# Optimization experiments

Measured on AMD Instinct MI355X. Metric: run time of the kernel, lower is better.

## Reference

```python
import jax, jax.numpy as jnp
import numpy as np

BS, S, D, H, KVH, HD = 2, 2048, 2048, 32, 8, 64
N_REP = H // KVH
N_DOCS = 4


def setup_inputs() -> dict:
    key = jax.random.key(0)
    ks = jax.random.split(key, 7)
    x = jax.random.normal(ks[0], (BS, S, D), dtype=jnp.float32)
    # RoPE table (llama theta=10000), stored as real (cos, sin) pairs: [S, HD//2, 2]
    inv_freq = 1.0 / (10000.0 ** (jnp.arange(0, HD, 2, dtype=jnp.float32) / HD))
    ang = jnp.arange(S, dtype=jnp.float32)[:, None] * inv_freq[None, :]  # [S, HD//2]
    freqs_cis = jnp.stack([jnp.cos(ang), jnp.sin(ang)], axis=-1)
    # packed-document ids, non-decreasing along sequence: [BS, S]
    sequence_id = jnp.sort(
        jax.random.randint(ks[1], (BS, S), 0, N_DOCS, dtype=jnp.int32), axis=-1
    )
    std = 0.02
    wq = jax.random.normal(ks[2], (H * HD, D), dtype=jnp.float32) * std
    wk = jax.random.normal(ks[3], (KVH * HD, D), dtype=jnp.float32) * std
    wv = jax.random.normal(ks[4], (KVH * HD, D), dtype=jnp.float32) * std
    wo = jax.random.normal(ks[5], (D, H * HD), dtype=jnp.float32) * std
    return {"x": x, "freqs_cis": freqs_cis, "sequence_id": sequence_id,
            "wq": wq, "wk": wk, "wv": wv, "wo": wo}


def _apply_rope(t, freqs_cis):
    # t: [b, s, h, hd]; freqs_cis: [s, hd//2, 2] (cos, sin)
    b, s, h, hd = t.shape
    tp = t.reshape(b, s, h, hd // 2, 2)
    t0, t1 = tp[..., 0], tp[..., 1]
    cos = freqs_cis[None, :, None, :, 0]
    sin = freqs_cis[None, :, None, :, 1]
    o0 = t0 * cos - t1 * sin
    o1 = t0 * sin + t1 * cos
    return jnp.stack([o0, o1], axis=-1).reshape(b, s, h, hd)


def reference(x, freqs_cis, sequence_id, wq, wk, wv, wo):
    bs, s, _ = x.shape
    xq = (x @ wq.T).reshape(bs, s, H, HD)
    xk = (x @ wk.T).reshape(bs, s, KVH, HD)
    xv = (x @ wv.T).reshape(bs, s, KVH, HD)
    xq = _apply_rope(xq, freqs_cis)
    xk = _apply_rope(xk, freqs_cis)
    # GQA without materializing repeated KV: group queries by kv head
    q = xq.reshape(bs, s, KVH, N_REP, HD).transpose(0, 2, 3, 1, 4)  # [b,g,r,s,d]
    k = xk.transpose(0, 2, 1, 3)  # [b,g,s,d]
    v = xv.transpose(0, 2, 1, 3)  # [b,g,s,d]
    scale = 1.0 / jnp.sqrt(jnp.float32(HD))
    scores = jnp.einsum("bgrqd,bgkd->bgrqk", q, k) * scale
    # document-causal mask: same sequence_id AND causal
    causal = jnp.tril(jnp.ones((s, s), dtype=bool))
    same_doc = sequence_id[:, :, None] == sequence_id[:, None, :]  # [b,s,s]
    mask = (causal[None] & same_doc)[:, None, None, :, :]  # [b,1,1,s,s]
    scores = jnp.where(mask, scores, jnp.float32(-1e30))
    probs = jax.nn.softmax(scores, axis=-1)
    out = jnp.einsum("bgrqk,bgkd->bgrqd", probs, v)  # [b,g,r,s,d]
    out = out.transpose(0, 3, 1, 2, 4).reshape(bs, s, H * HD)
    return out @ wo.T
```

## Files before the change

kernel.cpp:

```cpp
#include <hip/hip_runtime.h>
#include <hip/hip_bf16.h>

typedef __attribute__((ext_vector_type(8))) short bf16x8;
typedef __attribute__((ext_vector_type(4))) float f32x4;

#define MFMA16(A, B, C) __builtin_amdgcn_mfma_f32_16x16x32_bf16(A, B, C, 0, 0, 0)

__device__ __forceinline__ unsigned short f2bf(float f) {
    unsigned int u = __float_as_uint(f);
    u += 0x7fffu + ((u >> 16) & 1u);
    return (unsigned short)(u >> 16);
}
__device__ __forceinline__ float bf2f(unsigned short h) {
    return __uint_as_float(((unsigned int)h) << 16);
}
__device__ __forceinline__ unsigned int pack_bf2(float lo, float hi) {
    __hip_bfloat162 h = __float22bfloat162_rn(make_float2(lo, hi));
    return *reinterpret_cast<unsigned int*>(&h);
}

__device__ __forceinline__ void gload_lds16(const void* g, void* l) {
    __builtin_amdgcn_global_load_lds(
        (__attribute__((address_space(1))) unsigned int*)g,
        (__attribute__((address_space(3))) unsigned int*)l, 16, 0, 0);
}

__device__ __forceinline__ int swz128(int by) {
    return by ^ (((by >> 7) & 7) << 4);
}

__global__ void cvt_all_kernel(const float* __restrict__ x,  const float* __restrict__ wq,
                               const float* __restrict__ wk, const float* __restrict__ wv,
                               const float* __restrict__ wo,
                               unsigned short* __restrict__ xb,
                               unsigned short* __restrict__ wqkv,
                               unsigned short* __restrict__ wob) {
    const int i = blockIdx.x * 256 + threadIdx.x;
    const float* src;
    unsigned short* dst;
    int off;
    if (i < 2097152)      { src = x;  dst = xb;   off = i; }
    else if (i < 3145728) { src = wq; dst = wqkv; off = i - 2097152; }
    else if (i < 3407872) { src = wk; dst = wqkv + (size_t)2048 * 2048; off = i - 3145728; }
    else if (i < 3670016) { src = wv; dst = wqkv + (size_t)2560 * 2048; off = i - 3407872; }
    else                  { src = wo; dst = wob;  off = i - 3670016; }
    const float4 v = ((const float4*)src)[off];
    uint2 o;
    o.x = pack_bf2(v.x, v.y);
    o.y = pack_bf2(v.z, v.w);
    ((uint2*)dst)[off] = o;
}

__global__ void docstart_kernel(const int* __restrict__ sid, int* __restrict__ ds) {
    const int i = blockIdx.x * 256 + threadIdx.x;
    const int b = i >> 11, s = i & 2047;
    const int* row = sid + b * 2048;
    const int v = row[s];
    int lo = 0, hi = s;
    while (lo < hi) { const int mid = (lo + hi) >> 1; if (row[mid] < v) lo = mid + 1; else hi = mid; }
    ds[i] = lo;
}

#define QKV_K 2048
#define QKV_NT 32
__global__ __launch_bounds__(512, 2) void gemm_qkv8(
    const unsigned short* __restrict__ A,
    const unsigned short* __restrict__ B,
    unsigned short* __restrict__ oq,
    unsigned short* __restrict__ ok,
    unsigned short* __restrict__ ov)
{
    __shared__ __align__(16) unsigned short S[2][2][2][8192];
    const int tid = threadIdx.x, lane = tid & 63, w = tid >> 6;
    const int wr = w >> 2, wc = w & 3;
    const int lr = lane & 15, lc = lane >> 4;

    int bid = blockIdx.x;
    bid = (bid & 7) * 24 + (bid >> 3);
    const int m0 = (bid / 12) * 256, n0 = (bid % 12) * 256;

    const int o0 = (w << 11) + (lane << 4);
    const int o1 = o0 + 1024;
    const int v0 = swz128(o0), v1 = swz128(o1);
    const int r0 = v0 >> 7, c0 = (v0 & 127) >> 1;
    const int r1 = v1 >> 7, c1 = (v1 & 127) >> 1;
    const size_t aoff0 = (size_t)(m0 + r0) * QKV_K + c0;
    const size_t aoff1 = (size_t)(m0 + r1) * QKV_K + c1;
    const size_t boff0 = (size_t)(n0 + r0) * QKV_K + c0;
    const size_t boff1 = (size_t)(n0 + r1) * QKV_K + c1;
    const int d0 = o0 >> 1, d1 = o1 >> 1;

    f32x4 acc[2][2][4][2];
#pragma unroll
    for (int a = 0; a < 2; a++)
#pragma unroll
        for (int bq = 0; bq < 2; bq++)
#pragma unroll
            for (int i = 0; i < 4; i++)
#pragma unroll
                for (int j = 0; j < 2; j++) acc[a][bq][i][j] = (f32x4){0.f, 0.f, 0.f, 0.f};

    bf16x8 Af[4][2], Bf0[2][2], Bf1[2][2];

    auto STAGE_A = [&](int bf, int h, int kt) {
        gload_lds16(A + aoff0 + (size_t)h * 128 * QKV_K + (size_t)kt * 64, &S[bf][0][h][d0]);
        gload_lds16(A + aoff1 + (size_t)h * 128 * QKV_K + (size_t)kt * 64, &S[bf][0][h][d1]);
    };
    auto STAGE_B = [&](int bf, int h, int kt) {
        gload_lds16(B + boff0 + (size_t)h * 128 * QKV_K + (size_t)kt * 64, &S[bf][1][h][d0]);
        gload_lds16(B + boff1 + (size_t)h * 128 * QKV_K + (size_t)kt * 64, &S[bf][1][h][d1]);
    };
    auto LDA = [&](int bf, int mh) {
#pragma unroll
        for (int i = 0; i < 4; i++)
#pragma unroll
            for (int kh = 0; kh < 2; kh++) {
                const int by = swz128(((wr * 64 + i * 16 + lr) << 7) + (kh << 6) + (lc << 4));
                Af[i][kh] = *(const bf16x8*)((const char*)&S[bf][0][mh][0] + by);
            }
    };
    auto LDB = [&](int bf, int nh, bf16x8 (&Bf)[2][2]) {
#pragma unroll
        for (int j = 0; j < 2; j++)
#pragma unroll
            for (int kh = 0; kh < 2; kh++) {
                const int by = swz128(((wc * 32 + j * 16 + lr) << 7) + (kh << 6) + (lc << 4));
                Bf[j][kh] = *(const bf16x8*)((const char*)&S[bf][1][nh][0] + by);
            }
    };
    auto QUAD = [&](f32x4 (&ac)[4][2], bf16x8 (&Bf)[2][2]) {
        __builtin_amdgcn_s_setprio(1);
#pragma unroll
        for (int i = 0; i < 4; i++)
#pragma unroll
            for (int j = 0; j < 2; j++)
#pragma unroll
                for (int kh = 0; kh < 2; kh++)
                    ac[i][j] = MFMA16(Af[i][kh], Bf[j][kh], ac[i][j]);
        __builtin_amdgcn_s_setprio(0);
    };

#define BAR() __builtin_amdgcn_s_barrier()
#define LGKM0() asm volatile("s_waitcnt lgkmcnt(0)" ::: "memory")

    STAGE_A(0, 0, 0); STAGE_A(0, 1, 0); STAGE_B(0, 0, 0); STAGE_B(0, 1, 0);
    STAGE_A(1, 0, 1); STAGE_B(1, 1, 1); STAGE_A(1, 1, 1);
    asm volatile("s_waitcnt vmcnt(6)" ::: "memory");
    BAR();

    auto GROUP = [&](int g, int bf) {
        LDA(bf, 0); LDB(bf, 0, Bf0);
        if (g + 1 < QKV_NT) STAGE_B(bf ^ 1, 0, g + 1);
        BAR(); LGKM0();
        QUAD(acc[0][0], Bf0);
        BAR();
        LDB(bf, 1, Bf1);
        if (g + 2 < QKV_NT) STAGE_A(bf, 0, g + 2);
        BAR(); LGKM0();
        QUAD(acc[0][1], Bf1);
        BAR();
        LDA(bf, 1);
        if (g + 2 < QKV_NT) STAGE_B(bf, 1, g + 2);
        BAR(); LGKM0();
        QUAD(acc[1][1], Bf1);
        BAR();
        if (g + 2 < QKV_NT) STAGE_A(bf, 1, g + 2);
        BAR();
        QUAD(acc[1][0], Bf0);
        if (g == QKV_NT - 2) { asm volatile("s_waitcnt vmcnt(0)" ::: "memory"); }
        else                 { asm volatile("s_waitcnt vmcnt(6)" ::: "memory"); }
        BAR();
    };

#pragma unroll 1
    for (int g = 0; g < QKV_NT; g += 2) {
        GROUP(g, 0);
        GROUP(g + 1, 1);
    }

#pragma unroll
    for (int mh = 0; mh < 2; mh++)
#pragma unroll
        for (int nh = 0; nh < 2; nh++)
#pragma unroll
            for (int i = 0; i < 4; i++)
#pragma unroll
                for (int j = 0; j < 2; j++) {
                    const int n = n0 + nh * 128 + wc * 32 + j * 16 + lr;
                    const int d = n & 63;
                    const int hh6 = n >> 6;
#pragma unroll
                    for (int r = 0; r < 4; r++) {
                        const int m = m0 + mh * 128 + wr * 64 + i * 16 + lc * 4 + r;
                        const int bb = m >> 11, s = m & 2047;
                        const unsigned short val = f2bf(acc[mh][nh][i][j][r]);
                        if (n < 2048) {
                            oq[((((size_t)bb * 32 + hh6) * 2048 + s) << 6) + d] = val;
                        } else if (n < 2560) {
                            ok[((((size_t)bb * 8 + (hh6 - 32)) * 2048 + s) << 6) + d] = val;
                        } else {
                            ov[((((size_t)bb * 8 + (hh6 - 40)) * 2048 + s) << 6) + d] = val;
                        }
                    }
                }
}
#undef BAR
#undef LGKM0

__global__ void rope_kernel(unsigned short* __restrict__ Qb,
                            unsigned short* __restrict__ Kb,
                            const float* __restrict__ fc)
{
    const int NQ = 64 * 2048 * 8;
    int j = blockIdx.x * 256 + threadIdx.x;
    unsigned short* base;
    if (j < NQ) base = Qb;
    else { base = Kb; j -= NQ; }
    const int g = j & 7, s = (j >> 3) & 2047, bh = j >> 14;
    const size_t off = (((size_t)bh * 2048 + s) << 6) + g * 8;
    uint4 u = *(uint4*)&base[off];
    const float4 cs0 = *(const float4*)&fc[((s << 5) + g * 4) << 1];
    const float4 cs1 = *(const float4*)&fc[(((s << 5) + g * 4) << 1) + 4];
    unsigned int* uw = (unsigned int*)&u;
    float c[4] = {cs0.x, cs0.z, cs1.x, cs1.z};
    float sn[4] = {cs0.y, cs0.w, cs1.y, cs1.w};
#pragma unroll
    for (int q = 0; q < 4; q++) {
        const float t0 = bf2f((unsigned short)(uw[q] & 0xffffu));
        const float t1 = bf2f((unsigned short)(uw[q] >> 16));
        uw[q] = pack_bf2(fmaf(t0, c[q], -t1 * sn[q]), fmaf(t0, sn[q], t1 * c[q]));
    }
    *(uint4*)&base[off] = u;
}

template <int EPI>
__global__ __launch_bounds__(256) void gemm_bt(
    const unsigned short* __restrict__ A,
    const unsigned short* __restrict__ B,
    int K, int N,
    unsigned short* __restrict__ oq,
    unsigned short* __restrict__ ok,
    unsigned short* __restrict__ ov,
    float* __restrict__ of)
{
    __shared__ __align__(16) unsigned short sA[128 * 32];
    __shared__ __align__(16) unsigned short sB[128 * 32];
    const int tid = threadIdx.x;
    const int lane = tid & 63, wave = tid >> 6;
    const int wr = wave >> 1, wc = wave & 1;
    const int lr = lane & 15, lc = lane >> 4;

    int bid = blockIdx.y * gridDim.x + blockIdx.x;
    const int cpx = (gridDim.x * gridDim.y) >> 3;
    bid = (bid & 7) * cpx + (bid >> 3);
    const int m0 = (bid / gridDim.x) * 128, n0 = (bid % gridDim.x) * 128;

    f32x4 acc[4][4];
#pragma unroll
    for (int i = 0; i < 4; i++)
#pragma unroll
        for (int j = 0; j < 4; j++) acc[i][j] = (f32x4){0.f, 0.f, 0.f, 0.f};

    const int u0 = tid, u1 = tid + 256;
    for (int k0 = 0; k0 < K; k0 += 32) {
        __syncthreads();
        gload_lds16(A + (size_t)(m0 + (u0 >> 2)) * K + k0 + (u0 & 3) * 8, &sA[u0 * 8]);
        gload_lds16(A + (size_t)(m0 + (u1 >> 2)) * K + k0 + (u1 & 3) * 8, &sA[u1 * 8]);
        gload_lds16(B + (size_t)(n0 + (u0 >> 2)) * K + k0 + (u0 & 3) * 8, &sB[u0 * 8]);
        gload_lds16(B + (size_t)(n0 + (u1 >> 2)) * K + k0 + (u1 & 3) * 8, &sB[u1 * 8]);
        __syncthreads();
        bf16x8 af[4], bfv[4];
#pragma unroll
        for (int i = 0; i < 4; i++) {
            af[i]  = *(const bf16x8*)&sA[(wr * 64 + i * 16 + lr) * 32 + lc * 8];
            bfv[i] = *(const bf16x8*)&sB[(wc * 64 + i * 16 + lr) * 32 + lc * 8];
        }
#pragma unroll
        for (int i = 0; i < 4; i++)
#pragma unroll
            for (int j = 0; j < 4; j++) acc[i][j] = MFMA16(af[i], bfv[j], acc[i][j]);
    }

    if (EPI == 0) {
#pragma unroll
        for (int i = 0; i < 4; i++) {
#pragma unroll
            for (int j = 0; j < 4; j++) {
                const int n = n0 + wc * 64 + j * 16 + lr;
                const int d = n & 63;
#pragma unroll
                for (int r = 0; r < 4; r++) {
                    const int m = m0 + wr * 64 + i * 16 + lc * 4 + r;
                    const int bb = m >> 11, s = m & 2047;
                    const unsigned short val = f2bf(acc[i][j][r]);
                    if (n < 2048) {
                        const int hh = n >> 6;
                        oq[((((size_t)bb * 32 + hh) * 2048 + s) << 6) + d] = val;
                    } else if (n < 2560) {
                        const int hh = (n >> 6) - 32;
                        ok[((((size_t)bb * 8 + hh) * 2048 + s) << 6) + d] = val;
                    } else {
                        const int hh = (n >> 6) - 40;
                        ov[((((size_t)bb * 8 + hh) * 2048 + s) << 6) + d] = val;
                    }
                }
            }
        }
    } else {
#pragma unroll
        for (int i = 0; i < 4; i++)
#pragma unroll
            for (int j = 0; j < 4; j++)
#pragma unroll
                for (int r = 0; r < 4; r++) {
                    const int m = m0 + wr * 64 + i * 16 + lc * 4 + r;
                    const int n = n0 + wc * 64 + j * 16 + lr;
                    of[(size_t)m * N + n] = acc[i][j][r];
                }
    }
}

__global__ __launch_bounds__(512) void attn_kernel(
    const unsigned short* __restrict__ Q,
    const unsigned short* __restrict__ K,
    const unsigned short* __restrict__ V,
    const int* __restrict__ dstart,
    unsigned short* __restrict__ AO)
{
    const int qt = 15 - blockIdx.x;
    const int h = blockIdx.y, b = blockIdx.z;
    const int kvh = h >> 2;
    const int tid = threadIdx.x, lane = tid & 63, wave = tid >> 6;
    const int lr = lane & 15, lc = lane >> 4;
    const int q0 = qt * 128;
    const int qw = q0 + wave * 16;

    __shared__ __align__(16) unsigned short sK[2][64 * 64];
    __shared__ __align__(16) unsigned short sVt[2][64][72];

    const unsigned short* Qh = Q + (((size_t)b * 32 + h) * 2048) * 64;
    const unsigned short* Kh = K + (((size_t)b * 8 + kvh) * 2048) * 64;
    const unsigned short* Vh = V + (((size_t)b * 8 + kvh) * 2048) * 64;

    const bf16x8 qf0 = *(const bf16x8*)&Qh[(size_t)(qw + lr) * 64 + lc * 8];
    const bf16x8 qf1 = *(const bf16x8*)&Qh[(size_t)(qw + lr) * 64 + 32 + lc * 8];

    const int qglob = qw + lr;
    const int dsl = dstart[b * 2048 + qglob];
    const int ds_wmin = dstart[b * 2048 + qw];
    const int t0 = dstart[b * 2048 + q0] & ~63;

    const int w8 = wave * 8;
    const int kr = tid >> 3, kc = tid & 7;

    auto STAGE_K = [&](int t, int c) {
        gload_lds16(Kh + (size_t)(t + kr) * 64 + ((kc ^ (kr & 7)) * 8), &sK[c][tid * 8]);
    };
    auto WRITE_V = [&](const uint4& va, int c) {
        const unsigned short* pa = (const unsigned short*)&va;
#pragma unroll
        for (int e = 0; e < 8; e++) sVt[c][w8 + e][lane] = pa[e];
    };

    float mrow = -1e30f, lrow = 0.f;
    f32x4 oacc[4];
#pragma unroll
    for (int j = 0; j < 4; j++) oacc[j] = (f32x4){0.f, 0.f, 0.f, 0.f};

    STAGE_K(t0, 0);
    {
        const uint4 va = *(const uint4*)&Vh[(size_t)(t0 + lane) * 64 + w8];
        asm volatile("s_waitcnt vmcnt(0)" ::: "memory");
        WRITE_V(va, 0);
    }
    __syncthreads();

    int cb = 0;
    for (int t = t0; t < q0 + 128; t += 64, cb ^= 1) {
        const bool more = (t < q0 + 64);
        uint4 va;
        if (more) {
            STAGE_K(t + 64, cb ^ 1);
            va = *(const uint4*)&Vh[(size_t)(t + 64 + lane) * 64 + w8];
        }
        const bool act = !(t > qw + 15 || t + 63 < ds_wmin);
        union { unsigned int w[4]; bf16x8 v; } B0, B1;

        if (act) {
            f32x4 sc[4];
#pragma unroll
            for (int kk = 0; kk < 4; kk++) {
                const int krow = kk * 16 + lr;
                const bf16x8 kf0 = *(const bf16x8*)&sK[cb][krow * 64 + ((lc ^ (lr & 7)) * 8)];
                const bf16x8 kf1 = *(const bf16x8*)&sK[cb][krow * 64 + (((4 + lc) ^ (lr & 7)) * 8)];
                f32x4 a = (f32x4){0.f, 0.f, 0.f, 0.f};
                a = MFMA16(kf0, qf0, a);
                a = MFMA16(kf1, qf1, a);
                sc[kk] = a;
            }
            float vmax = -3e38f;
#pragma unroll
            for (int kk = 0; kk < 4; kk++)
#pragma unroll
                for (int r = 0; r < 4; r++) {
                    const int kpos = t + kk * 16 + lc * 4 + r;
                    const bool okm = (kpos <= qglob) && (kpos >= dsl);
                    sc[kk][r] = okm ? sc[kk][r] * 0.125f : -3e38f;
                    vmax = fmaxf(vmax, sc[kk][r]);
                }
            vmax = fmaxf(vmax, __shfl_xor(vmax, 16));
            vmax = fmaxf(vmax, __shfl_xor(vmax, 32));
            const float mnew = fmaxf(mrow, vmax);
            const float corr = __expf(mrow - mnew);
            mrow = mnew;

            float rsum = 0.f;
            unsigned int pk[4][2];
#pragma unroll
            for (int kk = 0; kk < 4; kk++) {
                const float p0 = __expf(sc[kk][0] - mnew);
                const float p1 = __expf(sc[kk][1] - mnew);
                const float p2 = __expf(sc[kk][2] - mnew);
                const float p3 = __expf(sc[kk][3] - mnew);
                rsum += (p0 + p1) + (p2 + p3);
                pk[kk][0] = pack_bf2(p0, p1);
                pk[kk][1] = pack_bf2(p2, p3);
            }
            rsum += __shfl_xor(rsum, 16);
            rsum += __shfl_xor(rsum, 32);
            lrow = lrow * corr + rsum;
#pragma unroll
            for (int j = 0; j < 4; j++)
#pragma unroll
                for (int r = 0; r < 4; r++) oacc[j][r] *= corr;

            const int srcEven = 32 * (lc & 1) + lr;
            const int srcOdd  = srcEven + 16;
            const bool hiKK = (lc & 2) != 0;
            unsigned int a, c;
            a = __shfl(pk[0][0], srcEven); c = __shfl(pk[1][0], srcEven); B0.w[0] = hiKK ? c : a;
            a = __shfl(pk[0][1], srcEven); c = __shfl(pk[1][1], srcEven); B0.w[1] = hiKK ? c : a;
            a = __shfl(pk[0][0], srcOdd);  c = __shfl(pk[1][0], srcOdd);  B0.w[2] = hiKK ? c : a;
            a = __shfl(pk[0][1], srcOdd);  c = __shfl(pk[1][1], srcOdd);  B0.w[3] = hiKK ? c : a;
            a = __shfl(pk[2][0], srcEven); c = __shfl(pk[3][0], srcEven); B1.w[0] = hiKK ? c : a;
            a = __shfl(pk[2][1], srcEven); c = __shfl(pk[3][1], srcEven); B1.w[1] = hiKK ? c : a;
            a = __shfl(pk[2][0], srcOdd);  c = __shfl(pk[3][0], srcOdd);  B1.w[2] = hiKK ? c : a;
            a = __shfl(pk[2][1], srcOdd);  c = __shfl(pk[3][1], srcOdd);  B1.w[3] = hiKK ? c : a;
        }

        if (more) {
            asm volatile("s_waitcnt vmcnt(0)" ::: "memory");
            WRITE_V(va, cb ^ 1);
        }

        if (act) {
#pragma unroll
            for (int j = 0; j < 4; j++) {
                const bf16x8 a0 = *(const bf16x8*)&sVt[cb][j * 16 + lr][lc * 8];
                const bf16x8 a1 = *(const bf16x8*)&sVt[cb][j * 16 + lr][32 + lc * 8];
                oacc[j] = MFMA16(a0, B0.v, oacc[j]);
                oacc[j] = MFMA16(a1, B1.v, oacc[j]);
            }
        }
        __syncthreads();
    }

    unsigned short (*E)[72] = (unsigned short (*)[72])&sVt[0][0][0];
    const float inv = 1.0f / lrow;
#pragma unroll
    for (int j = 0; j < 4; j++)
#pragma unroll
        for (int p = 0; p < 2; p++) {
            const unsigned int w = pack_bf2(oacc[j][2 * p] * inv, oacc[j][2 * p + 1] * inv);
            *(unsigned int*)&E[wave * 16 + lr][j * 16 + lc * 4 + 2 * p] = w;
        }
    __syncthreads();
#pragma unroll
    for (int half = 0; half < 2; half++) {
        const int c = lane + 64 * half;
        const int row = c >> 3, ch = c & 7;
        const uint4 o = *(const uint4*)&E[wave * 16 + row][ch * 8];
        *(uint4*)&AO[((size_t)b * 2048 + qw + row) * 2048 + h * 64 + ch * 8] = o;
    }
}

extern "C" void kernel_launch(void* const* d_in, const int* in_sizes, int n_in,
                              void* d_out, int out_size, void* d_ws, size_t ws_size,
                              hipStream_t stream) {
    const float* x  = (const float*)d_in[0];
    const float* fc = (const float*)d_in[1];
    const int* sid  = (const int*)d_in[2];
    const float* wq = (const float*)d_in[3];
    const float* wk = (const float*)d_in[4];
    const float* wv = (const float*)d_in[5];
    const float* wo = (const float*)d_in[6];
    float* out = (float*)d_out;

    unsigned short* xb   = (unsigned short*)d_ws;
    unsigned short* wqkv = xb + (size_t)4096 * 2048;
    unsigned short* wob  = wqkv + (size_t)3072 * 2048;
    unsigned short* Qb   = wob + (size_t)2048 * 2048;
    unsigned short* Kb   = Qb + (size_t)2 * 32 * 2048 * 64;
    unsigned short* Vb   = Kb + (size_t)2 * 8 * 2048 * 64;
    unsigned short* AO   = Vb + (size_t)2 * 8 * 2048 * 64;
    int* dstart = (int*)(AO + (size_t)4096 * 2048);

    cvt_all_kernel<<<18432, 256, 0, stream>>>(x, wq, wk, wv, wo, xb, wqkv, wob);
    docstart_kernel<<<16, 256, 0, stream>>>(sid, dstart);
    gemm_qkv8<<<dim3(192), 512, 0, stream>>>(xb, wqkv, Qb, Kb, Vb);
    rope_kernel<<<5120, 256, 0, stream>>>(Qb, Kb, fc);
    attn_kernel<<<dim3(16, 32, 2), 512, 0, stream>>>(Qb, Kb, Vb, dstart, AO);
    gemm_bt<1><<<dim3(16, 32), 256, 0, stream>>>(AO, wob, 2048, 2048, nullptr, nullptr, nullptr, out);
}
```

Before: 194.9 us.

## Swizzle GEMM LDS tiles, raise MFMA priority, use exp2 softmax with lazy rescale

The GEMM tile loader now XOR-swizzles the 16-byte chunk index both when filling LDS and when reading fragments, to cut LDS bank conflicts. s_setprio is raised around the MFMA blocks in both the GEMM and attention kernels. Attention folds log2(e) into the score scale so it can use exp2. It also skips the running-max rescale of the accumulators unless some row's max grows by more than 8 (log2 units). The lazy rescale leaves probabilities up to 2^8 before the bf16 pack, which costs some precision headroom and adds a wave vote per tile.

```diff
diff --git a/kernel.cpp b/kernel.cpp
--- a/kernel.cpp
+++ b/kernel.cpp
@@ -262,23 +262,28 @@
         for (int j = 0; j < 4; j++) acc[i][j] = (f32x4){0.f, 0.f, 0.f, 0.f};
 
     const int u0 = tid, u1 = tid + 256;
+    const int su0 = (u0 & 3) ^ ((u0 >> 3) & 3);
+    const int su1 = (u1 & 3) ^ ((u1 >> 3) & 3);
+    const int cX = (lc ^ ((lr >> 1) & 3)) * 8;
     for (int k0 = 0; k0 < K; k0 += 32) {
         __syncthreads();
-        gload_lds16(A + (size_t)(m0 + (u0 >> 2)) * K + k0 + (u0 & 3) * 8, &sA[u0 * 8]);
-        gload_lds16(A + (size_t)(m0 + (u1 >> 2)) * K + k0 + (u1 & 3) * 8, &sA[u1 * 8]);
-        gload_lds16(B + (size_t)(n0 + (u0 >> 2)) * K + k0 + (u0 & 3) * 8, &sB[u0 * 8]);
-        gload_lds16(B + (size_t)(n0 + (u1 >> 2)) * K + k0 + (u1 & 3) * 8, &sB[u1 * 8]);
+        gload_lds16(A + (size_t)(m0 + (u0 >> 2)) * K + k0 + su0 * 8, &sA[u0 * 8]);
+        gload_lds16(A + (size_t)(m0 + (u1 >> 2)) * K + k0 + su1 * 8, &sA[u1 * 8]);
+        gload_lds16(B + (size_t)(n0 + (u0 >> 2)) * K + k0 + su0 * 8, &sB[u0 * 8]);
+        gload_lds16(B + (size_t)(n0 + (u1 >> 2)) * K + k0 + su1 * 8, &sB[u1 * 8]);
         __syncthreads();
         bf16x8 af[4], bfv[4];
 #pragma unroll
         for (int i = 0; i < 4; i++) {
-            af[i]  = *(const bf16x8*)&sA[(wr * 64 + i * 16 + lr) * 32 + lc * 8];
-            bfv[i] = *(const bf16x8*)&sB[(wc * 64 + i * 16 + lr) * 32 + lc * 8];
-        }
+            af[i]  = *(const bf16x8*)&sA[(wr * 64 + i * 16 + lr) * 32 + cX];
+            bfv[i] = *(const bf16x8*)&sB[(wc * 64 + i * 16 + lr) * 32 + cX];
+        }
+        __builtin_amdgcn_s_setprio(1);
 #pragma unroll
         for (int i = 0; i < 4; i++)
 #pragma unroll
             for (int j = 0; j < 4; j++) acc[i][j] = MFMA16(af[i], bfv[j], acc[i][j]);
+        __builtin_amdgcn_s_setprio(0);
     }
 
     if (EPI == 0) {
@@ -362,6 +367,8 @@
         for (int e = 0; e < 8; e++) sVt[c][w8 + e][lane] = pa[e];
     };
 
+    const float SC2 = 0.125f * 1.4426950408889634f;
+
     float mrow = -1e30f, lrow = 0.f;
     f32x4 oacc[4];
 #pragma unroll
@@ -388,6 +395,7 @@
 
         if (act) {
             f32x4 sc[4];
+            __builtin_amdgcn_s_setprio(1);
 #pragma unroll
             for (int kk = 0; kk < 4; kk++) {
                 const int krow = kk * 16 + lr;
@@ -398,6 +406,7 @@
                 a = MFMA16(kf1, qf1, a);
                 sc[kk] = a;
             }
+            __builtin_amdgcn_s_setprio(0);
             float vmax = -3e38f;
 #pragma unroll
             for (int kk = 0; kk < 4; kk++)
@@ -405,34 +414,37 @@
                 for (int r = 0; r < 4; r++) {
                     const int kpos = t + kk * 16 + lc * 4 + r;
                     const bool okm = (kpos <= qglob) && (kpos >= dsl);
-                    sc[kk][r] = okm ? sc[kk][r] * 0.125f : -3e38f;
+                    sc[kk][r] = okm ? sc[kk][r] * SC2 : -3e38f;
                     vmax = fmaxf(vmax, sc[kk][r]);
                 }
             vmax = fmaxf(vmax, __shfl_xor(vmax, 16));
             vmax = fmaxf(vmax, __shfl_xor(vmax, 32));
-            const float mnew = fmaxf(mrow, vmax);
-            const float corr = __expf(mrow - mnew);
-            mrow = mnew;
+            if (!__all(vmax <= mrow + 8.f)) {
+                const float mnew = fmaxf(mrow, vmax);
+                const float corr = __builtin_exp2f(mrow - mnew);
+                mrow = mnew;
+                lrow *= corr;
+#pragma unroll
+                for (int j = 0; j < 4; j++)
+#pragma unroll
+                    for (int r = 0; r < 4; r++) oacc[j][r] *= corr;
+            }
 
             float rsum = 0.f;
             unsigned int pk[4][2];
 #pragma unroll
             for (int kk = 0; kk < 4; kk++) {
-                const float p0 = __expf(sc[kk][0] - mnew);
-                const float p1 = __expf(sc[kk][1] - mnew);
-                const float p2 = __expf(sc[kk][2] - mnew);
-                const float p3 = __expf(sc[kk][3] - mnew);
+                const float p0 = __builtin_exp2f(sc[kk][0] - mrow);
+                const float p1 = __builtin_exp2f(sc[kk][1] - mrow);
+                const float p2 = __builtin_exp2f(sc[kk][2] - mrow);
+                const float p3 = __builtin_exp2f(sc[kk][3] - mrow);
                 rsum += (p0 + p1) + (p2 + p3);
                 pk[kk][0] = pack_bf2(p0, p1);
                 pk[kk][1] = pack_bf2(p2, p3);
             }
             rsum += __shfl_xor(rsum, 16);
             rsum += __shfl_xor(rsum, 32);
-            lrow = lrow * corr + rsum;
-#pragma unroll
-            for (int j = 0; j < 4; j++)
-#pragma unroll
-                for (int r = 0; r < 4; r++) oacc[j][r] *= corr;
+            lrow += rsum;
 
             const int srcEven = 32 * (lc & 1) + lr;
             const int srcOdd  = srcEven + 16;
@@ -454,6 +466,7 @@
         }
 
         if (act) {
+            __builtin_amdgcn_s_setprio(1);
 #pragma unroll
             for (int j = 0; j < 4; j++) {
                 const bf16x8 a0 = *(const bf16x8*)&sVt[cb][j * 16 + lr][lc * 8];
@@ -461,6 +474,7 @@
                 oacc[j] = MFMA16(a0, B0.v, oacc[j]);
                 oacc[j] = MFMA16(a1, B1.v, oacc[j]);
             }
+            __builtin_amdgcn_s_setprio(0);
         }
         __syncthreads();
     }
```

After: 199.6 us. 2.4% more time.
